# Kernel optimization log

Measured on AMD Instinct MI355X. Metric: run time of the kernel, lower is better.

Reference implementation:

```python
import jax, jax.numpy as jnp
import numpy as np

D_MODEL = 1024
N_HEADS = 16
HEAD_DIM = D_MODEL // N_HEADS
B, LQ, LK = 4, 2048, 2048


def _rope(x, cos, sin):
    # x: (B, H, L, d); cos/sin: (B, 1, L, d)
    d = x.shape[-1]
    x1, x2 = x[..., : d // 2], x[..., d // 2 :]
    rotated = jnp.concatenate([-x2, x1], axis=-1)
    return x * cos + rotated * sin


def setup_inputs() -> dict:
    key = jax.random.key(0)
    ks = jax.random.split(key, 16)
    s = 1.0 / np.sqrt(D_MODEL)
    inp = {
        "query": jax.random.normal(ks[0], (B, LQ, D_MODEL), jnp.float32),
        "key": jax.random.normal(ks[1], (B, LK, D_MODEL), jnp.float32),
        "value": jax.random.normal(ks[2], (B, LK, D_MODEL), jnp.float32),
        "cos_q": jax.random.normal(ks[3], (B, LQ, HEAD_DIM), jnp.float32),
        "sin_q": jax.random.normal(ks[4], (B, LQ, HEAD_DIM), jnp.float32),
        "cos_k": jax.random.normal(ks[5], (B, LK, HEAD_DIM), jnp.float32),
        "sin_k": jax.random.normal(ks[6], (B, LK, HEAD_DIM), jnp.float32),
        "key_padding_mask": jnp.zeros((B, LK), dtype=bool),
        "Wq": jax.random.normal(ks[7], (D_MODEL, D_MODEL), jnp.float32) * s,
        "bq": jnp.zeros((D_MODEL,), jnp.float32),
        "Wk": jax.random.normal(ks[8], (D_MODEL, D_MODEL), jnp.float32) * s,
        "bk": jnp.zeros((D_MODEL,), jnp.float32),
        "Wv": jax.random.normal(ks[9], (D_MODEL, D_MODEL), jnp.float32) * s,
        "bv": jnp.zeros((D_MODEL,), jnp.float32),
        "Wo": jax.random.normal(ks[10], (D_MODEL, D_MODEL), jnp.float32) * s,
        "bo": jnp.zeros((D_MODEL,), jnp.float32),
    }
    return inp


def reference(query, key, value, cos_q, sin_q, cos_k, sin_k, key_padding_mask,
              Wq, bq, Wk, bk, Wv, bv, Wo, bo):
    Bq, Lq, _ = query.shape
    Lk = key.shape[1]
    scale = HEAD_DIM ** -0.5

    def proj(x, W, b, L):
        # torch Linear: x @ W.T + b, then (B, L, H, d) -> (B, H, L, d)
        y = jnp.einsum('ble,de->bld', x, W) + b
        return y.reshape(Bq, L, N_HEADS, HEAD_DIM).transpose(0, 2, 1, 3)

    q = proj(query, Wq, bq, Lq)
    k = proj(key, Wk, bk, Lk)
    v = proj(value, Wv, bv, Lk)

    q = _rope(q, cos_q[:, None, :Lq, :HEAD_DIM], sin_q[:, None, :Lq, :HEAD_DIM])
    k = _rope(k, cos_k[:, None, :Lk, :HEAD_DIM], sin_k[:, None, :Lk, :HEAD_DIM])

    attn = jnp.einsum('bhqd,bhkd->bhqk', q, k) * scale
    attn = jnp.where(key_padding_mask[:, None, None, :], -jnp.inf, attn)
    attn = jax.nn.softmax(attn, axis=-1)

    out = jnp.einsum('bhqk,bhkd->bhqd', attn, v)
    out = out.transpose(0, 2, 1, 3).reshape(Bq, Lq, D_MODEL)
    return jnp.einsum('ble,de->bld', out, Wo) + bo
```

## Files before the change

kernel.cpp:

```cpp
#include <hip/hip_runtime.h>
#include <hip/hip_bf16.h>
#include <stdint.h>
#include <stddef.h>

#define B_DIM 4
#define NH    16
#define LSEQ  2048
#define HD    64
#define DM    1024
#define TOKENS (B_DIM * LSEQ)

typedef __bf16 bf16_t;
typedef __attribute__((ext_vector_type(8))) __bf16 bf16x8;
typedef __attribute__((ext_vector_type(4))) __bf16 bf16x4;
typedef __attribute__((ext_vector_type(4))) float  f32x4;

#define GLD16(gp, lp) \
  __builtin_amdgcn_global_load_lds((__attribute__((address_space(1))) void*)(gp), \
                                   (__attribute__((address_space(3))) void*)(lp), 16, 0, 0)

__device__ __forceinline__ f32x4 mfma_16x16x32(bf16x8 a, bf16x8 b, f32x4 c) {
  return __builtin_amdgcn_mfma_f32_16x16x32_bf16(a, b, c, 0, 0, 0);
}

__global__ __launch_bounds__(256) void cast3_kernel(const float* __restrict__ a,
                                                    const float* __restrict__ b,
                                                    const float* __restrict__ c,
                                                    bf16_t* __restrict__ dst, int n) {
  const float* src = (blockIdx.y == 0) ? a : (blockIdx.y == 1) ? b : c;
  const int i = (blockIdx.x * 256 + threadIdx.x) * 4;
  if (i < n) {
    const float4 v = *(const float4*)(src + i);
    bf16x4 o;
    o[0] = (bf16_t)v.x; o[1] = (bf16_t)v.y; o[2] = (bf16_t)v.z; o[3] = (bf16_t)v.w;
    *(bf16x4*)(dst + (size_t)blockIdx.y * n + i) = o;
  }
}

__global__ __launch_bounds__(256) void cast4_kernel(const float* __restrict__ a,
                                                    const float* __restrict__ b,
                                                    const float* __restrict__ c,
                                                    const float* __restrict__ d,
                                                    bf16_t* __restrict__ dst, int n) {
  const float* src = (blockIdx.y == 0) ? a : (blockIdx.y == 1) ? b
                   : (blockIdx.y == 2) ? c : d;
  const int i = (blockIdx.x * 256 + threadIdx.x) * 4;
  if (i < n) {
    const float4 v = *(const float4*)(src + i);
    bf16x4 o;
    o[0] = (bf16_t)v.x; o[1] = (bf16_t)v.y; o[2] = (bf16_t)v.z; o[3] = (bf16_t)v.w;
    *(bf16x4*)(dst + (size_t)blockIdx.y * n + i) = o;
  }
}

__global__ __launch_bounds__(256) void qkv_proj_kernel(const bf16_t* __restrict__ X,
                                                       const bf16_t* __restrict__ Wb,
                                                       const float* __restrict__ bq,
                                                       const float* __restrict__ bk,
                                                       const float* __restrict__ bv,
                                                       const float* __restrict__ cos_q,
                                                       const float* __restrict__ sin_q,
                                                       const float* __restrict__ cos_k,
                                                       const float* __restrict__ sin_k,
                                                       bf16_t* __restrict__ qtb,
                                                       bf16_t* __restrict__ ktb,
                                                       bf16_t* __restrict__ vtb) {
  __shared__ bf16_t As[2][128 * 32];
  __shared__ bf16_t Bs[2][128 * 32];
  const int z = blockIdx.z;
  const bf16_t* A  = X  + (size_t)z * TOKENS * DM;
  const bf16_t* Bw = Wb + (size_t)z * DM * DM;
  const float* bias = (z == 0) ? bq : (z == 1) ? bk : bv;

  const int tid  = threadIdx.x;
  const int wave = tid >> 6, lane = tid & 63;
  const int quad = lane >> 4, l16 = lane & 15;
  const int m0 = blockIdx.x * 128, n0 = blockIdx.y * 128;
  const int wm = (wave >> 1) * 64, wn = (wave & 1) * 64;

  f32x4 acc[4][4];
#pragma unroll
  for (int i = 0; i < 4; ++i)
#pragma unroll
    for (int j = 0; j < 4; ++j) acc[i][j] = (f32x4){0.f, 0.f, 0.f, 0.f};

  const int srow = lane >> 2;
  const int scol = ((lane & 3) ^ ((lane >> 3) & 3)) * 8;
  const int c0 = wave * 2, c1 = c0 + 1;
  const int r0 = c0 * 16 + srow, r1 = c1 * 16 + srow;
  const bf16_t* Ag0 = A  + (size_t)(m0 + r0) * DM + scol;
  const bf16_t* Ag1 = A  + (size_t)(m0 + r1) * DM + scol;
  const bf16_t* Bg0 = Bw + (size_t)(n0 + r0) * DM + scol;
  const bf16_t* Bg1 = Bw + (size_t)(n0 + r1) * DM + scol;
  const int ld0 = c0 * 512, ld1 = c1 * 512;

  const int fcol = ((quad ^ ((l16 >> 1) & 3)) << 3);

  GLD16(Ag0, &As[0][0] + ld0); GLD16(Ag1, &As[0][0] + ld1);
  GLD16(Bg0, &Bs[0][0] + ld0); GLD16(Bg1, &Bs[0][0] + ld1);
  __syncthreads();

  int cur = 0;
  for (int t = 0; t < 32; ++t) {
    if (t < 31) {
      const int kk = (t + 1) * 32;
      bf16_t* Ad = &As[cur ^ 1][0];
      bf16_t* Bd = &Bs[cur ^ 1][0];
      GLD16(Ag0 + kk, Ad + ld0); GLD16(Ag1 + kk, Ad + ld1);
      GLD16(Bg0 + kk, Bd + ld0); GLD16(Bg1 + kk, Bd + ld1);
    }
    const bf16_t* Ac = &As[cur][0];
    const bf16_t* Bc = &Bs[cur][0];
    bf16x8 af[4], bfr[4];
#pragma unroll
    for (int i = 0; i < 4; ++i)
      af[i] = *(const bf16x8*)(Ac + (wm + i * 16 + l16) * 32 + fcol);
#pragma unroll
    for (int j = 0; j < 4; ++j)
      bfr[j] = *(const bf16x8*)(Bc + (wn + j * 16 + l16) * 32 + fcol);
#pragma unroll
    for (int i = 0; i < 4; ++i)
#pragma unroll
      for (int j = 0; j < 4; ++j)
        acc[i][j] = mfma_16x16x32(af[i], bfr[j], acc[i][j]);
    if (t < 31) __syncthreads();
    cur ^= 1;
  }

  if (z < 2) {
    const float* cosb = (z == 0) ? cos_q : cos_k;
    const float* sinb = (z == 0) ? sin_q : sin_k;
    bf16_t* out = (z == 0) ? qtb : ktb;
    const int h = (n0 + wn) >> 6;
#pragma unroll
    for (int i = 0; i < 4; ++i) {
#pragma unroll
      for (int j = 0; j < 2; ++j) {
        const int hd1 = j * 16 + l16;
        const int hd2 = hd1 + 32;
        const float bn1 = bias[n0 + wn + hd1];
        const float bn2 = bias[n0 + wn + hd2];
#pragma unroll
        for (int r = 0; r < 4; ++r) {
          const int m = m0 + wm + i * 16 + quad * 4 + r;
          const int b = m >> 11, l = m & (LSEQ - 1);
          const size_t cb = ((size_t)b * LSEQ + l) * HD;
          const float x1 = (float)(bf16_t)(acc[i][j][r] + bn1);
          const float x2 = (float)(bf16_t)(acc[i][j + 2][r] + bn2);
          const float c1 = cosb[cb + hd1], s1 = sinb[cb + hd1];
          const float c2 = cosb[cb + hd2], s2 = sinb[cb + hd2];
          bf16_t* dst = out + (((size_t)(b * NH + h)) * LSEQ + l) * HD;
          dst[hd1] = (bf16_t)(x1 * c1 - x2 * s1);
          dst[hd2] = (bf16_t)(x2 * c2 + x1 * s2);
        }
      }
    }
  } else {
#pragma unroll
    for (int i = 0; i < 4; ++i) {
      const int mb = m0 + wm + i * 16 + quad * 4;
      const int b = mb >> 11, l = mb & (LSEQ - 1);
#pragma unroll
      for (int j = 0; j < 4; ++j) {
        const int n = n0 + wn + j * 16 + l16;
        const int h = n >> 6, hd = n & (HD - 1);
        const float bn = bias[n];
        bf16x4 pk;
#pragma unroll
        for (int r = 0; r < 4; ++r) pk[r] = (bf16_t)(acc[i][j][r] + bn);
        *(bf16x4*)(vtb + (((size_t)(b * NH + h)) * HD + hd) * LSEQ + l) = pk;
      }
    }
  }
}

__global__ __launch_bounds__(256) void out_gemm_kernel(const bf16_t* __restrict__ A,
                                                       const bf16_t* __restrict__ Bw,
                                                       const float* __restrict__ bias,
                                                       float* __restrict__ out) {
  __shared__ bf16_t As[2][128 * 32];
  __shared__ bf16_t Bs[2][128 * 32];
  const int tid  = threadIdx.x;
  const int wave = tid >> 6, lane = tid & 63;
  const int quad = lane >> 4, l16 = lane & 15;
  const int m0 = blockIdx.x * 128, n0 = blockIdx.y * 128;
  const int wm = (wave >> 1) * 64, wn = (wave & 1) * 64;

  f32x4 acc[4][4];
#pragma unroll
  for (int i = 0; i < 4; ++i)
#pragma unroll
    for (int j = 0; j < 4; ++j) acc[i][j] = (f32x4){0.f, 0.f, 0.f, 0.f};

  const int srow = lane >> 2;
  const int scol = ((lane & 3) ^ ((lane >> 3) & 3)) * 8;
  const int c0 = wave * 2, c1 = c0 + 1;
  const int r0 = c0 * 16 + srow, r1 = c1 * 16 + srow;
  const bf16_t* Ag0 = A  + (size_t)(m0 + r0) * DM + scol;
  const bf16_t* Ag1 = A  + (size_t)(m0 + r1) * DM + scol;
  const bf16_t* Bg0 = Bw + (size_t)(n0 + r0) * DM + scol;
  const bf16_t* Bg1 = Bw + (size_t)(n0 + r1) * DM + scol;
  const int ld0 = c0 * 512, ld1 = c1 * 512;
  const int fcol = ((quad ^ ((l16 >> 1) & 3)) << 3);

  GLD16(Ag0, &As[0][0] + ld0); GLD16(Ag1, &As[0][0] + ld1);
  GLD16(Bg0, &Bs[0][0] + ld0); GLD16(Bg1, &Bs[0][0] + ld1);
  __syncthreads();

  int cur = 0;
  for (int t = 0; t < 32; ++t) {
    if (t < 31) {
      const int kk = (t + 1) * 32;
      bf16_t* Ad = &As[cur ^ 1][0];
      bf16_t* Bd = &Bs[cur ^ 1][0];
      GLD16(Ag0 + kk, Ad + ld0); GLD16(Ag1 + kk, Ad + ld1);
      GLD16(Bg0 + kk, Bd + ld0); GLD16(Bg1 + kk, Bd + ld1);
    }
    const bf16_t* Ac = &As[cur][0];
    const bf16_t* Bc = &Bs[cur][0];
    bf16x8 af[4], bfr[4];
#pragma unroll
    for (int i = 0; i < 4; ++i)
      af[i] = *(const bf16x8*)(Ac + (wm + i * 16 + l16) * 32 + fcol);
#pragma unroll
    for (int j = 0; j < 4; ++j)
      bfr[j] = *(const bf16x8*)(Bc + (wn + j * 16 + l16) * 32 + fcol);
#pragma unroll
    for (int i = 0; i < 4; ++i)
#pragma unroll
      for (int j = 0; j < 4; ++j)
        acc[i][j] = mfma_16x16x32(af[i], bfr[j], acc[i][j]);
    if (t < 31) __syncthreads();
    cur ^= 1;
  }

#pragma unroll
  for (int i = 0; i < 4; ++i)
#pragma unroll
    for (int j = 0; j < 4; ++j) {
      const int n  = n0 + wn + j * 16 + l16;
      const float bn = bias[n];
#pragma unroll
      for (int r = 0; r < 4; ++r) {
        const int m = m0 + wm + i * 16 + quad * 4 + r;
        out[(size_t)m * DM + n] = acc[i][j][r] + bn;
      }
    }
}

__global__ __launch_bounds__(256, 4) void attn_kernel(const bf16_t* __restrict__ qt,
                                                      const bf16_t* __restrict__ kt,
                                                      const bf16_t* __restrict__ vt,
                                                      const unsigned char* __restrict__ mask,
                                                      bf16_t* __restrict__ ctx) {
  __shared__ bf16_t Kl[2][64 * 64];
  __shared__ bf16_t Vl[2][64 * 64];
  __shared__ int mflag;
  const int bh = blockIdx.y;
  const int b = bh >> 4, h = bh & (NH - 1);
  const int q0 = blockIdx.x * 128;
  const int tid = threadIdx.x;
  const int wave = tid >> 6, lane = tid & 63;
  const int quad = lane >> 4, l16 = lane & 15;
  const float scale_l2e = 0.125f * 1.44269504f;

  const bf16_t* kbase = kt + (size_t)bh * LSEQ * HD;
  const bf16_t* vbase = vt + (size_t)bh * HD * LSEQ;
  const unsigned char* mrow = mask + (size_t)b * LSEQ;

  if (tid == 0) mflag = 0;
  __syncthreads();
  {
    const uint64_t mw = ((const uint64_t*)mrow)[tid];
    if (mw != 0) atomicOr(&mflag, 1);
  }

  bf16x8 qa[2][2];
#pragma unroll
  for (int u = 0; u < 2; ++u) {
    const bf16_t* qrow = qt + (((size_t)bh * LSEQ) + q0 + wave * 32 + u * 16 + l16) * HD;
    qa[u][0] = *(const bf16x8*)(qrow + quad * 8);
    qa[u][1] = *(const bf16x8*)(qrow + 32 + quad * 8);
  }

  f32x4 O[2][4];
  f32x4 Ol[2];
#pragma unroll
  for (int u = 0; u < 2; ++u) {
    Ol[u] = (f32x4){0.f, 0.f, 0.f, 0.f};
#pragma unroll
    for (int j = 0; j < 4; ++j) O[u][j] = (f32x4){0.f, 0.f, 0.f, 0.f};
  }
  bf16x8 ones;
#pragma unroll
  for (int e = 0; e < 8; ++e) ones[e] = (bf16_t)1.0f;

  const int srow8 = lane >> 3;
  const int scb   = lane & 7;
  const int c0 = wave * 2, c1 = c0 + 1;
  const int p0 = c0 * 8 + srow8, p1 = p0 + 8;
  const int g0 = (scb ^ srow8) * 8;
  const int sig0 = ((p0 >> 5) << 5) | (((p0 >> 2) & 3) << 3) | (((p0 >> 4) & 1) << 2) | (p0 & 3);
  const int sig1 = ((p1 >> 5) << 5) | (((p1 >> 2) & 3) << 3) | (((p1 >> 4) & 1) << 2) | (p1 & 3);
  const int kgo0 = sig0 * HD + g0, kgo1 = sig1 * HD + g0;
  const int vgo0 = p0 * LSEQ + g0, vgo1 = p1 * LSEQ + g0;
  const int ld0 = c0 * 512, ld1 = c1 * 512;

  const int sw  = l16 & 7;
  const int oA  = l16 * 64 + ((quad ^ sw) << 3);
  const int oB  = l16 * 64 + (((quad + 4) ^ sw) << 3);

  GLD16(kbase + kgo0, &Kl[0][0] + ld0);
  GLD16(kbase + kgo1, &Kl[0][0] + ld1);
  GLD16(vbase + vgo0, &Vl[0][0] + ld0);
  GLD16(vbase + vgo1, &Vl[0][0] + ld1);
  __syncthreads();
  const bool has_mask = (mflag != 0);

  int cur = 0;
  for (int t = 0; t < 32; ++t) {
    const int k0 = t * 64;

    if (t < 31) {
      const int k0n = k0 + 64;
      bf16_t* Kd = &Kl[cur ^ 1][0];
      bf16_t* Vd = &Vl[cur ^ 1][0];
      GLD16(kbase + (size_t)k0n * HD + kgo0, Kd + ld0);
      GLD16(kbase + (size_t)k0n * HD + kgo1, Kd + ld1);
      GLD16(vbase + (size_t)(vgo0 + k0n), Vd + ld0);
      GLD16(vbase + (size_t)(vgo1 + k0n), Vd + ld1);
    }

    const bf16_t* Kc = &Kl[cur][0];
    const bf16_t* Vc = &Vl[cur][0];

    f32x4 S[2][4];
#pragma unroll
    for (int j = 0; j < 4; ++j) {
      const bf16x8 kb0 = *(const bf16x8*)(Kc + oA + j * 1024);
      const bf16x8 kb1 = *(const bf16x8*)(Kc + oB + j * 1024);
#pragma unroll
      for (int u = 0; u < 2; ++u) {
        f32x4 a = (f32x4){0.f, 0.f, 0.f, 0.f};
        a = mfma_16x16x32(kb0, qa[u][0], a);
        a = mfma_16x16x32(kb1, qa[u][1], a);
#pragma unroll
        for (int r = 0; r < 4; ++r)
          S[u][j][r] = __builtin_amdgcn_exp2f(a[r] * scale_l2e);
      }
    }

    if (has_mask) {
      const uint64_t mlo = *(const uint64_t*)(mrow + k0 + quad * 8);
      const uint64_t mhi = *(const uint64_t*)(mrow + k0 + 32 + quad * 8);
      if (!__all((mlo | mhi) == 0)) {
#pragma unroll
        for (int j = 0; j < 4; ++j) {
          const uint64_t mm = (j & 2) ? mhi : mlo;
#pragma unroll
          for (int r = 0; r < 4; ++r)
            if ((mm >> (((j & 1) * 4 + r) * 8)) & 0xff) {
              S[0][j][r] = 0.f;
              S[1][j][r] = 0.f;
            }
        }
      }
    }

    bf16x8 pa[2][2];
#pragma unroll
    for (int u = 0; u < 2; ++u)
#pragma unroll
      for (int f = 0; f < 2; ++f)
#pragma unroll
        for (int e = 0; e < 8; ++e)
          pa[u][f][e] = (bf16_t)S[u][2 * f + (e >> 2)][e & 3];

#pragma unroll
    for (int u = 0; u < 2; ++u) {
      Ol[u] = mfma_16x16x32(pa[u][0], ones, Ol[u]);
      Ol[u] = mfma_16x16x32(pa[u][1], ones, Ol[u]);
    }

#pragma unroll
    for (int jd = 0; jd < 4; ++jd) {
      const bf16x8 vb0 = *(const bf16x8*)(Vc + oA + jd * 1024);
      const bf16x8 vb1 = *(const bf16x8*)(Vc + oB + jd * 1024);
#pragma unroll
      for (int u = 0; u < 2; ++u) {
        O[u][jd] = mfma_16x16x32(pa[u][0], vb0, O[u][jd]);
        O[u][jd] = mfma_16x16x32(pa[u][1], vb1, O[u][jd]);
      }
    }

    if (t < 31) __syncthreads();
    cur ^= 1;
  }

#pragma unroll
  for (int u = 0; u < 2; ++u) {
    f32x4 linv;
#pragma unroll
    for (int r = 0; r < 4; ++r) linv[r] = 1.0f / Ol[u][r];
#pragma unroll
    for (int jd = 0; jd < 4; ++jd)
#pragma unroll
      for (int r = 0; r < 4; ++r) {
        const int l = q0 + wave * 32 + u * 16 + quad * 4 + r;
        const int d = h * HD + jd * 16 + l16;
        const float o = O[u][jd][r] * linv[r];
        ctx[((size_t)b * LSEQ + l) * DM + d] = (bf16_t)o;
      }
  }
}

extern "C" void kernel_launch(void* const* d_in, const int* in_sizes, int n_in,
                              void* d_out, int out_size, void* d_ws, size_t ws_size,
                              hipStream_t stream) {
  (void)in_sizes; (void)n_in; (void)out_size; (void)ws_size;
  const float* query = (const float*)d_in[0];
  const float* key   = (const float*)d_in[1];
  const float* value = (const float*)d_in[2];
  const float* cos_q = (const float*)d_in[3];
  const float* sin_q = (const float*)d_in[4];
  const float* cos_k = (const float*)d_in[5];
  const float* sin_k = (const float*)d_in[6];
  const unsigned char* mask = (const unsigned char*)d_in[7];
  const float* Wq = (const float*)d_in[8];
  const float* bq = (const float*)d_in[9];
  const float* Wk = (const float*)d_in[10];
  const float* bk = (const float*)d_in[11];
  const float* Wv = (const float*)d_in[12];
  const float* bv = (const float*)d_in[13];
  const float* Wo = (const float*)d_in[14];
  const float* bo = (const float*)d_in[15];
  float* out = (float*)d_out;

  const size_t ACT = (size_t)TOKENS * DM;
  const size_t WEL = (size_t)DM * DM;

  bf16_t* p   = (bf16_t*)d_ws;
  bf16_t* xq  = p; p += ACT;
  bf16_t* xk  = p; p += ACT;
  bf16_t* xv  = p; p += ACT;
  bf16_t* wqb = p; p += WEL;
  bf16_t* wkb = p; p += WEL;
  bf16_t* wvb = p; p += WEL;
  bf16_t* wob = p; p += WEL;
  bf16_t* qtb = p; p += ACT;
  bf16_t* ktb = p; p += ACT;
  bf16_t* vtb = p; p += ACT;
  bf16_t* ctx = xk;
  (void)xv; (void)wkb; (void)wvb;

  cast3_kernel<<<dim3((int)(ACT / 1024), 3), 256, 0, stream>>>(query, key, value, xq, (int)ACT);
  cast4_kernel<<<dim3((int)(WEL / 1024), 4), 256, 0, stream>>>(Wq, Wk, Wv, Wo, wqb, (int)WEL);

  qkv_proj_kernel<<<dim3(TOKENS / 128, DM / 128, 3), 256, 0, stream>>>(
      xq, wqb, bq, bk, bv, cos_q, sin_q, cos_k, sin_k, qtb, ktb, vtb);

  attn_kernel<<<dim3(LSEQ / 128, B_DIM * NH), 256, 0, stream>>>(qtb, ktb, vtb, mask, ctx);

  out_gemm_kernel<<<dim3(TOKENS / 128, DM / 128), 256, 0, stream>>>(ctx, wob, bo, out);
}
```

Measured before the change: 367.2 us.

## Pipeline GEMM global-to-LDS loads with partial vmcnt waits across two buffers

Replaces the simple double-buffered K loop in the QKV and output projection GEMMs with a software pipeline. Two tiles of loads stay in flight, and explicit s_waitcnt vmcnt(4) lets each step wait only for the older tile before its barrier. After compute, the buffer just consumed is refilled with the tile two steps ahead, so global latency overlaps with more MFMA work instead of draining each iteration. It relies on hand-placed waitcnt, barriers and sched_barrier being correct, which risks races if the counting is off.

```diff
diff --git a/kernel.cpp b/kernel.cpp
--- a/kernel.cpp
+++ b/kernel.cpp
@@ -18,6 +18,12 @@
 #define GLD16(gp, lp) \
   __builtin_amdgcn_global_load_lds((__attribute__((address_space(1))) void*)(gp), \
                                    (__attribute__((address_space(3))) void*)(lp), 16, 0, 0)
+
+#define WAITV4 asm volatile("s_waitcnt vmcnt(4)" ::: "memory")
+#define WAITV0 asm volatile("s_waitcnt vmcnt(0)" ::: "memory")
+#define WAITL0 asm volatile("s_waitcnt lgkmcnt(0)" ::: "memory")
+#define SBAR   __builtin_amdgcn_s_barrier()
+#define SCHED0 __builtin_amdgcn_sched_barrier(0)
 
 __device__ __forceinline__ f32x4 mfma_16x16x32(bf16x8 a, bf16x8 b, f32x4 c) {
   return __builtin_amdgcn_mfma_f32_16x16x32_bf16(a, b, c, 0, 0, 0);
@@ -52,6 +58,29 @@
     *(bf16x4*)(dst + (size_t)blockIdx.y * n + i) = o;
   }
 }
+
+#define GEMM_TILE(CUR, WAIT, PRE, KK2)                                        \
+  {                                                                           \
+    WAIT; SBAR; SCHED0;                                                       \
+    const bf16_t* Ac = &As[CUR][0];                                           \
+    const bf16_t* Bc = &Bs[CUR][0];                                           \
+    bf16x8 af[4], bfr[4];                                                     \
+    _Pragma("unroll") for (int i_ = 0; i_ < 4; ++i_)                          \
+      af[i_] = *(const bf16x8*)(Ac + (wm + i_ * 16 + l16) * 32 + fcol);       \
+    _Pragma("unroll") for (int j_ = 0; j_ < 4; ++j_)                          \
+      bfr[j_] = *(const bf16x8*)(Bc + (wn + j_ * 16 + l16) * 32 + fcol);      \
+    _Pragma("unroll") for (int i_ = 0; i_ < 4; ++i_)                          \
+      _Pragma("unroll") for (int j_ = 0; j_ < 4; ++j_)                        \
+        acc[i_][j_] = mfma_16x16x32(af[i_], bfr[j_], acc[i_][j_]);            \
+    WAITL0; SBAR; SCHED0;                                                     \
+    if (PRE) {                                                                \
+      const int kk2_ = (KK2);                                                 \
+      GLD16(Ag0 + kk2_, &As[CUR][0] + ld0);                                   \
+      GLD16(Ag1 + kk2_, &As[CUR][0] + ld1);                                   \
+      GLD16(Bg0 + kk2_, &Bs[CUR][0] + ld0);                                   \
+      GLD16(Bg1 + kk2_, &Bs[CUR][0] + ld1);                                   \
+    }                                                                         \
+  }
 
 __global__ __launch_bounds__(256) void qkv_proj_kernel(const bf16_t* __restrict__ X,
                                                        const bf16_t* __restrict__ Wb,
@@ -98,34 +127,16 @@
 
   GLD16(Ag0, &As[0][0] + ld0); GLD16(Ag1, &As[0][0] + ld1);
   GLD16(Bg0, &Bs[0][0] + ld0); GLD16(Bg1, &Bs[0][0] + ld1);
-  __syncthreads();
-
-  int cur = 0;
-  for (int t = 0; t < 32; ++t) {
-    if (t < 31) {
-      const int kk = (t + 1) * 32;
-      bf16_t* Ad = &As[cur ^ 1][0];
-      bf16_t* Bd = &Bs[cur ^ 1][0];
-      GLD16(Ag0 + kk, Ad + ld0); GLD16(Ag1 + kk, Ad + ld1);
-      GLD16(Bg0 + kk, Bd + ld0); GLD16(Bg1 + kk, Bd + ld1);
-    }
-    const bf16_t* Ac = &As[cur][0];
-    const bf16_t* Bc = &Bs[cur][0];
-    bf16x8 af[4], bfr[4];
-#pragma unroll
-    for (int i = 0; i < 4; ++i)
-      af[i] = *(const bf16x8*)(Ac + (wm + i * 16 + l16) * 32 + fcol);
-#pragma unroll
-    for (int j = 0; j < 4; ++j)
-      bfr[j] = *(const bf16x8*)(Bc + (wn + j * 16 + l16) * 32 + fcol);
-#pragma unroll
-    for (int i = 0; i < 4; ++i)
-#pragma unroll
-      for (int j = 0; j < 4; ++j)
-        acc[i][j] = mfma_16x16x32(af[i], bfr[j], acc[i][j]);
-    if (t < 31) __syncthreads();
-    cur ^= 1;
-  }
+  GLD16(Ag0 + 32, &As[1][0] + ld0); GLD16(Ag1 + 32, &As[1][0] + ld1);
+  GLD16(Bg0 + 32, &Bs[1][0] + ld0); GLD16(Bg1 + 32, &Bs[1][0] + ld1);
+
+  for (int ii = 0; ii < 15; ++ii) {
+    const int kk2a = ii * 64 + 64;
+    GEMM_TILE(0, WAITV4, true, kk2a);
+    GEMM_TILE(1, WAITV4, true, kk2a + 32);
+  }
+  GEMM_TILE(0, WAITV4, false, 0);
+  GEMM_TILE(1, WAITV0, false, 0);
 
   if (z < 2) {
     const float* cosb = (z == 0) ? cos_q : cos_k;
@@ -205,34 +216,16 @@
 
   GLD16(Ag0, &As[0][0] + ld0); GLD16(Ag1, &As[0][0] + ld1);
   GLD16(Bg0, &Bs[0][0] + ld0); GLD16(Bg1, &Bs[0][0] + ld1);
-  __syncthreads();
-
-  int cur = 0;
-  for (int t = 0; t < 32; ++t) {
-    if (t < 31) {
-      const int kk = (t + 1) * 32;
-      bf16_t* Ad = &As[cur ^ 1][0];
-      bf16_t* Bd = &Bs[cur ^ 1][0];
-      GLD16(Ag0 + kk, Ad + ld0); GLD16(Ag1 + kk, Ad + ld1);
-      GLD16(Bg0 + kk, Bd + ld0); GLD16(Bg1 + kk, Bd + ld1);
-    }
-    const bf16_t* Ac = &As[cur][0];
-    const bf16_t* Bc = &Bs[cur][0];
-    bf16x8 af[4], bfr[4];
-#pragma unroll
-    for (int i = 0; i < 4; ++i)
-      af[i] = *(const bf16x8*)(Ac + (wm + i * 16 + l16) * 32 + fcol);
-#pragma unroll
-    for (int j = 0; j < 4; ++j)
-      bfr[j] = *(const bf16x8*)(Bc + (wn + j * 16 + l16) * 32 + fcol);
-#pragma unroll
-    for (int i = 0; i < 4; ++i)
-#pragma unroll
-      for (int j = 0; j < 4; ++j)
-        acc[i][j] = mfma_16x16x32(af[i], bfr[j], acc[i][j]);
-    if (t < 31) __syncthreads();
-    cur ^= 1;
-  }
+  GLD16(Ag0 + 32, &As[1][0] + ld0); GLD16(Ag1 + 32, &As[1][0] + ld1);
+  GLD16(Bg0 + 32, &Bs[1][0] + ld0); GLD16(Bg1 + 32, &Bs[1][0] + ld1);
+
+  for (int ii = 0; ii < 15; ++ii) {
+    const int kk2a = ii * 64 + 64;
+    GEMM_TILE(0, WAITV4, true, kk2a);
+    GEMM_TILE(1, WAITV4, true, kk2a + 32);
+  }
+  GEMM_TILE(0, WAITV4, false, 0);
+  GEMM_TILE(1, WAITV0, false, 0);
 
 #pragma unroll
   for (int i = 0; i < 4; ++i)
```

After: 359.9 us. 1.02x faster.
